# Kernel optimization log

Measured on AMD Instinct MI355X. Metric: run time of the kernel, lower is better.

## Reference

```python
import jax, jax.numpy as jnp
import numpy as np

N_EMBD = 1024
HEAD_SIZE = 64

def setup_inputs() -> dict:
    key = jax.random.key(0)
    kx, kk, kq, kv = jax.random.split(key, 4)
    x = jax.random.normal(kx, (8, 2048, N_EMBD), dtype=jnp.float32)
    # torch nn.Linear(n_embd, head_size, bias=False): y = x @ W.T, W:[head_size,n_embd].
    # We store the transposed form [n_embd, head_size] directly.
    s = 1.0 / np.sqrt(N_EMBD)
    Wk = jax.random.uniform(kk, (N_EMBD, HEAD_SIZE), jnp.float32, -s, s)
    Wq = jax.random.uniform(kq, (N_EMBD, HEAD_SIZE), jnp.float32, -s, s)
    Wv = jax.random.uniform(kv, (N_EMBD, HEAD_SIZE), jnp.float32, -s, s)
    return {"x": x, "Wk": Wk, "Wq": Wq, "Wv": Wv}

def reference(x, Wk, Wq, Wv):
    B, T, C = x.shape
    k = jnp.einsum('btc,cd->btd', x, Wk)  # [B,T,d]
    q = jnp.einsum('btc,cd->btd', x, Wq)
    v = jnp.einsum('btc,cd->btd', x, Wv)
    d = k.shape[-1]
    wei = jnp.einsum('btd,bsd->bts', q, k) * (d ** -0.5)  # [B,T,T]
    causal = jnp.tril(jnp.ones((T, T), dtype=bool))
    wei = jnp.where(causal, wei, -jnp.inf)
    wei = jax.nn.softmax(wei, axis=-1)
    # dropout p=0.0 -> identity (eval-mode equivalent)
    out = jnp.einsum('bts,bsd->btd', wei, v)  # [B,T,d]
    return out
```

## Files before the change

kernel.cpp:

```cpp
#include <hip/hip_runtime.h>
#include <hip/hip_bf16.h>

#define TB 8
#define TT 2048
#define TC 1024
#define TD 64
#define PSP 72

typedef __attribute__((ext_vector_type(8))) short bf16x8;
typedef __attribute__((ext_vector_type(4))) float f32x4;

__device__ __forceinline__ short f2bf(float f) {
    union { float f; unsigned u; } v; v.f = f;
    unsigned r = v.u + 0x7fffu + ((v.u >> 16) & 1u);
    return (short)(r >> 16);
}

__device__ __forceinline__ unsigned pk2(float a, float b) {
    __hip_bfloat162 h = __float22bfloat162_rn(make_float2(a, b));
    union { __hip_bfloat162 h2; unsigned u; } c; c.h2 = h;
    return c.u;
}

__device__ __forceinline__ void gl_lds16(const void* g, void* l) {
    __builtin_amdgcn_global_load_lds(
        (const __attribute__((address_space(1))) unsigned*)g,
        (__attribute__((address_space(3))) unsigned*)l, 16, 0, 0);
}

__device__ __forceinline__ void bar_raw() { asm volatile("s_barrier" ::: "memory"); }
#define WAIT_VM(n) asm volatile("s_waitcnt vmcnt(" #n ")" ::: "memory")

__global__ __launch_bounds__(256) void convert_w(const float* __restrict__ Wk,
                                                 const float* __restrict__ Wq,
                                                 const float* __restrict__ Wv,
                                                 short* __restrict__ Wt) {
    __shared__ short Tl[64 * PSP];
    const int tid = threadIdx.x;
    const int kc  = blockIdx.x;
    const int oid = blockIdx.y;
    const float* src = (oid == 0) ? Wk : (oid == 1) ? Wq : Wv;
    const float scale = (oid == 1) ? 0.125f : 1.0f;
    const int row = tid >> 2;
    const int c0  = (tid & 3) << 4;

    const float* sp = src + (size_t)(kc * 64 + row) * TD + c0;
    float4 a = ((const float4*)sp)[0], b = ((const float4*)sp)[1];
    float4 c = ((const float4*)sp)[2], d = ((const float4*)sp)[3];
    float vals[16] = {a.x,a.y,a.z,a.w, b.x,b.y,b.z,b.w,
                      c.x,c.y,c.z,c.w, d.x,d.y,d.z,d.w};
#pragma unroll
    for (int j = 0; j < 16; ++j)
        Tl[(c0 + j) * PSP + row] = f2bf(vals[j] * scale);
    __syncthreads();

    const int n  = tid >> 2;
    const int k0 = (tid & 3) << 4;
    uint4 u0 = *(uint4*)&Tl[n * PSP + k0];
    uint4 u1 = *(uint4*)&Tl[n * PSP + k0 + 8];
    uint4* dst = (uint4*)(Wt + (size_t)(oid * 64 + n) * TC + kc * 64 + k0);
    dst[0] = u0; dst[1] = u1;
}

__global__ __launch_bounds__(256, 1) void qkv_proj(const float* __restrict__ x,
                                                   const short* __restrict__ Wt,
                                                   short* __restrict__ qb,
                                                   short* __restrict__ kb,
                                                   short* __restrict__ vt) {
    __shared__ __align__(16) char sm[3 * 40960];
    const int tid = threadIdx.x;
    const int mg  = blockIdx.x;
    const int wv  = tid >> 6, lane = tid & 63;
    const int wu  = __builtin_amdgcn_readfirstlane(wv);
    const int l15 = lane & 15, quad = lane >> 4;

    f32x4 acc[12];
#pragma unroll
    for (int i = 0; i < 12; ++i) acc[i] = (f32x4){0.f, 0.f, 0.f, 0.f};

    const float* xtile = x + (size_t)mg * 64 * TC;

#define STAGE_Q(r)                                                          \
    {                                                                       \
        char* sb = sm + ((r) % 3) * 40960;                                  \
        float* xd = (float*)sb;                                             \
        short* wd = (short*)(sb + 16384);                                   \
        _Pragma("unroll")                                                   \
        for (int j = 0; j < 4; ++j) {                                       \
            int sbase = (j * 4 + wu) * 64;                                  \
            int sl = sbase + lane;                                          \
            int rw = sl >> 4, g = sl & 15;                                  \
            int gg = g ^ (rw & 15);                                         \
            gl_lds16(xtile + (size_t)rw * TC + (r) * 64 + gg * 4,           \
                     xd + (size_t)sbase * 4);                               \
        }                                                                   \
        _Pragma("unroll")                                                   \
        for (int j = 0; j < 6; ++j) {                                       \
            int n0 = (j * 4 + wu) * 8;                                      \
            int nb = n0 + (lane >> 3), g = lane & 7;                        \
            int gg = g ^ (nb & 7);                                          \
            gl_lds16(Wt + (size_t)nb * TC + (r) * 64 + gg * 8,              \
                     wd + (size_t)n0 * 64);                                 \
        }                                                                   \
    }

    STAGE_Q(0);
    STAGE_Q(1);
    for (int r = 0; r < 16; ++r) {
        if (r + 2 < 16)      { STAGE_Q(r + 2); WAIT_VM(20); }
        else if (r + 1 < 16) { WAIT_VM(10); }
        else                 { WAIT_VM(0); }
        bar_raw();
        const char* sb = sm + (r % 3) * 40960;
        const float* xb = (const float*)sb;
        const short* wb = (const short*)(sb + 16384);
        const int xrow = (wv * 16 + l15) * 16;
#pragma unroll
        for (int c = 0; c < 2; ++c) {
            int G = c * 8 + quad * 2;
            float4 f0 = *(const float4*)(xb + (xrow + (G ^ l15)) * 4);
            float4 f1 = *(const float4*)(xb + (xrow + ((G + 1) ^ l15)) * 4);
            union { bf16x8 v; unsigned u[4]; } pk;
            pk.u[0] = pk2(f0.x, f0.y); pk.u[1] = pk2(f0.z, f0.w);
            pk.u[2] = pk2(f1.x, f1.y); pk.u[3] = pk2(f1.z, f1.w);
#pragma unroll
            for (int nt = 0; nt < 12; ++nt) {
                bf16x8 B = *(const bf16x8*)(wb + (nt * 16 + l15) * 64
                                            + (((c * 4 + quad) ^ (l15 & 7)) * 8));
                acc[nt] = __builtin_amdgcn_mfma_f32_16x16x32_bf16(pk.v, B, acc[nt], 0, 0, 0);
            }
        }
        bar_raw();
    }
#undef STAGE_Q

    const int row0 = mg * 64;
    const int bb = row0 >> 11;
    const int m0 = wv * 16 + quad * 4;
#pragma unroll
    for (int nt = 0; nt < 4; ++nt)
#pragma unroll
        for (int rr = 0; rr < 4; ++rr)
            kb[(size_t)(row0 + m0 + rr) * TD + nt * 16 + l15] = f2bf(acc[nt][rr]);
#pragma unroll
    for (int nt = 4; nt < 8; ++nt)
#pragma unroll
        for (int rr = 0; rr < 4; ++rr)
            qb[(size_t)(row0 + m0 + rr) * TD + (nt - 4) * 16 + l15] = f2bf(acc[nt][rr]);
#pragma unroll
    for (int nt = 8; nt < 12; ++nt) {
        int d = (nt - 8) * 16 + l15;
        alignas(8) short t4[4];
#pragma unroll
        for (int rr = 0; rr < 4; ++rr) t4[rr] = f2bf(acc[nt][rr]);
        *(uint2*)(vt + (size_t)(bb * TD + d) * TT + (row0 & 2047) + m0) = *(uint2*)t4;
    }
}

__global__ __launch_bounds__(256, 1) void attn(const short* __restrict__ qb,
                                               const short* __restrict__ kb,
                                               const short* __restrict__ vt,
                                               float* __restrict__ out) {
    __shared__ __align__(16) char smem[107520];
    short* Ps = (short*)(smem + 98304);
    float* Os = (float*)smem;
    float* ls = (float*)(smem + 16384);

    const int tid = threadIdx.x;
    const int p   = blockIdx.x;
    const int b   = blockIdx.y;
    const int wv  = tid >> 6, lane = tid & 63;
    const int wu  = __builtin_amdgcn_readfirstlane(wv);
    const int l15 = lane & 15, quad = lane >> 4;
    const int qh  = wv >> 1;
    const int ks  = wv & 1;
    const float L2E = 1.4426950408889634f;

    const short* kbb = kb + (size_t)b * TT * TD;
    const short* vbb = vt + (size_t)b * TD * TT;
    short* myPs = Ps + wu * (16 * PSP);
    const int col = tid & 63;
    const int rb  = tid >> 6;

#define STAGE_KV(r, KTv)                                                    \
    {                                                                       \
        char* sb = smem + ((r) % 3) * 32768;                                \
        short* kdst = (short*)sb;                                           \
        short* vdst = (short*)(sb + 16384);                                 \
        _Pragma("unroll")                                                   \
        for (int h = 0; h < 2; ++h) {                                       \
            int kt = 2 * (r) + h; if (kt > (KTv) - 1) kt = (KTv) - 1;       \
            _Pragma("unroll")                                               \
            for (int j = 0; j < 2; ++j) {                                   \
                int sbase = (j * 4 + wu) * 64;                              \
                int sl = sbase + lane;                                      \
                int rw = sl >> 3, g = sl & 7;                               \
                int gg = g ^ (rw & 7);                                      \
                gl_lds16(kbb + (size_t)(kt * 64 + rw) * TD + gg * 8,        \
                         kdst + h * 4096 + sbase * 8);                      \
                gl_lds16(vbb + (size_t)rw * TT + kt * 64 + gg * 8,          \
                         vdst + h * 4096 + sbase * 8);                      \
            }                                                               \
        }                                                                   \
    }

    for (int phase = 0; phase < 2; ++phase) {
        const int it = phase ? (63 - p) : p;
        const int q0 = it * 32;
        const int KT = (it >> 1) + 1;
        const int R  = (KT + 1) >> 1;

        const size_t qoff = (size_t)(b * TT + q0 + qh * 16 + l15) * TD + quad * 8;
        bf16x8 aq0 = *(const bf16x8*)(qb + qoff);
        bf16x8 aq1 = *(const bf16x8*)(qb + qoff + 32);
        WAIT_VM(0);

        f32x4 O[4];
#pragma unroll
        for (int i = 0; i < 4; ++i) O[i] = (f32x4){0.f, 0.f, 0.f, 0.f};
        float lsum[4] = {0.f, 0.f, 0.f, 0.f};

        STAGE_KV(0, KT);
        if (1 < R) STAGE_KV(1, KT);
        for (int r = 0; r < R; ++r) {
            if (r + 2 < R)      { STAGE_KV(r + 2, KT); WAIT_VM(16); }
            else if (r + 1 < R) { WAIT_VM(8); }
            else                { WAIT_VM(0); }
            bar_raw();

            const int mykt = 2 * r + ks;
            if (mykt < KT) {
                const char* sb2 = (const char*)smem + (r % 3) * 32768;
                const short* Kt = (const short*)sb2 + ks * 4096;
                const short* Vt = (const short*)(sb2 + 16384) + ks * 4096;
                f32x4 S[4];
#pragma unroll
                for (int nt = 0; nt < 4; ++nt) {
                    int rw = nt * 16 + l15, r7 = l15 & 7;
                    bf16x8 b0 = *(const bf16x8*)(Kt + rw * 64 + (quad ^ r7) * 8);
                    bf16x8 b1 = *(const bf16x8*)(Kt + rw * 64 + ((4 + quad) ^ r7) * 8);
                    S[nt] = (f32x4){0.f, 0.f, 0.f, 0.f};
                    S[nt] = __builtin_amdgcn_mfma_f32_16x16x32_bf16(aq0, b0, S[nt], 0, 0, 0);
                    S[nt] = __builtin_amdgcn_mfma_f32_16x16x32_bf16(aq1, b1, S[nt], 0, 0, 0);
                }
                const bool diag = (mykt == KT - 1);
                const int qrow = q0 + qh * 16 + quad * 4;
#pragma unroll
                for (int nt = 0; nt < 4; ++nt) {
                    int scol = mykt * 64 + nt * 16 + l15;
#pragma unroll
                    for (int r4 = 0; r4 < 4; ++r4) {
                        float pv = exp2f(S[nt][r4] * L2E);
                        if (diag && (scol > qrow + r4)) pv = 0.f;
                        lsum[r4] += pv;
                        myPs[(quad * 4 + r4) * PSP + nt * 16 + l15] = f2bf(pv);
                    }
                }
                bf16x8 p0 = *(const bf16x8*)(myPs + l15 * PSP + quad * 8);
                bf16x8 p1 = *(const bf16x8*)(myPs + l15 * PSP + quad * 8 + 32);
#pragma unroll
                for (int dt = 0; dt < 4; ++dt) {
                    int rw = dt * 16 + l15, r7 = l15 & 7;
                    bf16x8 b0 = *(const bf16x8*)(Vt + rw * 64 + (quad ^ r7) * 8);
                    bf16x8 b1 = *(const bf16x8*)(Vt + rw * 64 + ((4 + quad) ^ r7) * 8);
                    O[dt] = __builtin_amdgcn_mfma_f32_16x16x32_bf16(p0, b0, O[dt], 0, 0, 0);
                    O[dt] = __builtin_amdgcn_mfma_f32_16x16x32_bf16(p1, b1, O[dt], 0, 0, 0);
                }
            }
            bar_raw();
        }
        __syncthreads();

#pragma unroll
        for (int r = 0; r < 4; ++r) {
            float v = lsum[r];
            v += __shfl_xor(v, 1); v += __shfl_xor(v, 2);
            v += __shfl_xor(v, 4); v += __shfl_xor(v, 8);
            lsum[r] = v;
        }
#pragma unroll
        for (int dt = 0; dt < 4; ++dt)
#pragma unroll
            for (int r = 0; r < 4; ++r)
                Os[(wv * 16 + quad * 4 + r) * 64 + dt * 16 + l15] = O[dt][r];
        if (l15 == 0)
#pragma unroll
            for (int r = 0; r < 4; ++r) ls[wv * 16 + quad * 4 + r] = lsum[r];
        __syncthreads();

        for (int rr = rb; rr < 32; rr += 4) {
            int h = rr >> 4, r16 = rr & 15;
            float o = Os[((2 * h)     * 16 + r16) * 64 + col]
                    + Os[((2 * h + 1) * 16 + r16) * 64 + col];
            float L = ls[(2 * h) * 16 + r16] + ls[(2 * h + 1) * 16 + r16];
            out[(size_t)(b * TT + q0 + rr) * TD + col] = o / L;
        }
        __syncthreads();
    }
#undef STAGE_KV
}

extern "C" void kernel_launch(void* const* d_in, const int* in_sizes, int n_in,
                              void* d_out, int out_size, void* d_ws, size_t ws_size,
                              hipStream_t stream) {
    const float* x  = (const float*)d_in[0];
    const float* Wk = (const float*)d_in[1];
    const float* Wq = (const float*)d_in[2];
    const float* Wv = (const float*)d_in[3];
    float* out = (float*)d_out;

    char* ws = (char*)d_ws;
    short* Wt = (short*)(ws);
    short* qb = (short*)(ws + 524288);
    short* kb = (short*)(ws + 2621440);
    short* vt = (short*)(ws + 4718592);

    convert_w<<<dim3(16, 3), dim3(256), 0, stream>>>(Wk, Wq, Wv, Wt);
    qkv_proj<<<dim3(256), dim3(256), 0, stream>>>(x, Wt, qb, kb, vt);
    attn<<<dim3(32, 8), dim3(256), 0, stream>>>(qb, kb, vt, out);
}
```

Before: 141.0 us.

## Restructure attention to one 64-row query tile per block, retile QKV warps

The attention kernel drops the paired-phase, split-K-across-waves scheme. Each block now handles one 64-query tile, with each wave owning 16 rows and the whole KV range. The separate LDS reduction of partial O and row sums goes away, and results are written directly to global memory. LDS use shrinks so two blocks can share a CU, and heavy tiles are scheduled first. The QKV projection switches to a 2x2 wave tiling, 32 rows by 6 n-tiles, so each B fragment is reused across two M tiles. It also gains a redundant first store loop with an odd index expression.

```diff
diff --git a/kernel.cpp b/kernel.cpp
--- a/kernel.cpp
+++ b/kernel.cpp
@@ -73,10 +73,14 @@
     const int wv  = tid >> 6, lane = tid & 63;
     const int wu  = __builtin_amdgcn_readfirstlane(wv);
     const int l15 = lane & 15, quad = lane >> 4;
-
-    f32x4 acc[12];
-#pragma unroll
-    for (int i = 0; i < 12; ++i) acc[i] = (f32x4){0.f, 0.f, 0.f, 0.f};
+    const int mh  = wv >> 1;
+    const int nh  = wv & 1;
+
+    f32x4 acc[2][6];
+#pragma unroll
+    for (int i = 0; i < 2; ++i)
+#pragma unroll
+        for (int j = 0; j < 6; ++j) acc[i][j] = (f32x4){0.f, 0.f, 0.f, 0.f};
 
     const float* xtile = x + (size_t)mg * 64 * TC;
 
@@ -114,190 +118,183 @@
         const char* sb = sm + (r % 3) * 40960;
         const float* xb = (const float*)sb;
         const short* wb = (const short*)(sb + 16384);
-        const int xrow = (wv * 16 + l15) * 16;
 #pragma unroll
         for (int c = 0; c < 2; ++c) {
             int G = c * 8 + quad * 2;
-            float4 f0 = *(const float4*)(xb + (xrow + (G ^ l15)) * 4);
-            float4 f1 = *(const float4*)(xb + (xrow + ((G + 1) ^ l15)) * 4);
-            union { bf16x8 v; unsigned u[4]; } pk;
-            pk.u[0] = pk2(f0.x, f0.y); pk.u[1] = pk2(f0.z, f0.w);
-            pk.u[2] = pk2(f1.x, f1.y); pk.u[3] = pk2(f1.z, f1.w);
-#pragma unroll
-            for (int nt = 0; nt < 12; ++nt) {
-                bf16x8 B = *(const bf16x8*)(wb + (nt * 16 + l15) * 64
-                                            + (((c * 4 + quad) ^ (l15 & 7)) * 8));
-                acc[nt] = __builtin_amdgcn_mfma_f32_16x16x32_bf16(pk.v, B, acc[nt], 0, 0, 0);
+#pragma unroll
+            for (int mt = 0; mt < 2; ++mt) {
+                const int xrow = (mh * 32 + mt * 16 + l15) * 16;
+                float4 f0 = *(const float4*)(xb + (xrow + (G ^ l15)) * 4);
+                float4 f1 = *(const float4*)(xb + (xrow + ((G + 1) ^ l15)) * 4);
+                union { bf16x8 v; unsigned u[4]; } pk;
+                pk.u[0] = pk2(f0.x, f0.y); pk.u[1] = pk2(f0.z, f0.w);
+                pk.u[2] = pk2(f1.x, f1.y); pk.u[3] = pk2(f1.z, f1.w);
+#pragma unroll
+                for (int i = 0; i < 6; ++i) {
+                    int nt = nh * 6 + i;
+                    bf16x8 B = *(const bf16x8*)(wb + (nt * 16 + l15) * 64
+                                                + (((c * 4 + quad) ^ (l15 & 7)) * 8));
+                    acc[mt][i] = __builtin_amdgcn_mfma_f32_16x16x32_bf16(
+                                     pk.v, B, acc[mt][i], 0, 0, 0);
+                }
             }
         }
         bar_raw();
     }
 #undef STAGE_Q
 
-    const int row0 = mg * 64;
-    const int bb = row0 >> 11;
-    const int m0 = wv * 16 + quad * 4;
-#pragma unroll
-    for (int nt = 0; nt < 4; ++nt)
-#pragma unroll
-        for (int rr = 0; rr < 4; ++rr)
-            kb[(size_t)(row0 + m0 + rr) * TD + nt * 16 + l15] = f2bf(acc[nt][rr]);
-#pragma unroll
-    for (int nt = 4; nt < 8; ++nt)
-#pragma unroll
-        for (int rr = 0; rr < 4; ++rr)
-            qb[(size_t)(row0 + m0 + rr) * TD + (nt - 4) * 16 + l15] = f2bf(acc[nt][rr]);
-#pragma unroll
-    for (int nt = 8; nt < 12; ++nt) {
-        int d = (nt - 8) * 16 + l15;
-        alignas(8) short t4[4];
-#pragma unroll
-        for (int rr = 0; rr < 4; ++rr) t4[rr] = f2bf(acc[nt][rr]);
-        *(uint2*)(vt + (size_t)(bb * TD + d) * TT + (row0 & 2047) + m0) = *(uint2*)t4;
-    }
-}
-
-__global__ __launch_bounds__(256, 1) void attn(const short* __restrict__ qb,
+    const int row0 = mg * 64 + mh * 32;
+    const int bb = mg >> 5;
+#pragma unroll
+    for (int i = 0; i < 6; ++i) {
+        int nt = nh * 6 + i;
+        if (nt < 4) {
+#pragma unroll
+            for (int mt = 0; mt < 2; ++mt)
+#pragma unroll
+                for (int rr = 0; rr < 4; ++rr)
+                    kb[(size_t)(row0 + mt * 16 + quad * 4 + rr) * TD + nt * 16 + l15]
+                        = f2bf(acc[mt][rr >> 2 ? 0 : i][rr]);
+        }
+    }
+#pragma unroll
+    for (int i = 0; i < 6; ++i) {
+        int nt = nh * 6 + i;
+#pragma unroll
+        for (int mt = 0; mt < 2; ++mt) {
+            if (nt < 4) {
+#pragma unroll
+                for (int rr = 0; rr < 4; ++rr)
+                    kb[(size_t)(row0 + mt * 16 + quad * 4 + rr) * TD + nt * 16 + l15]
+                        = f2bf(acc[mt][i][rr]);
+            } else if (nt < 8) {
+#pragma unroll
+                for (int rr = 0; rr < 4; ++rr)
+                    qb[(size_t)(row0 + mt * 16 + quad * 4 + rr) * TD + (nt - 4) * 16 + l15]
+                        = f2bf(acc[mt][i][rr]);
+            } else {
+                int d = (nt - 8) * 16 + l15;
+                alignas(8) short t4[4];
+#pragma unroll
+                for (int rr = 0; rr < 4; ++rr) t4[rr] = f2bf(acc[mt][i][rr]);
+                *(uint2*)(vt + (size_t)(bb * TD + d) * TT
+                          + ((row0 + mt * 16) & 2047) + quad * 4) = *(uint2*)t4;
+            }
+        }
+    }
+}
+
+__global__ __launch_bounds__(256, 2) void attn(const short* __restrict__ qb,
                                                const short* __restrict__ kb,
                                                const short* __restrict__ vt,
                                                float* __restrict__ out) {
-    __shared__ __align__(16) char smem[107520];
-    short* Ps = (short*)(smem + 98304);
-    float* Os = (float*)smem;
-    float* ls = (float*)(smem + 16384);
+    __shared__ __align__(16) char smem[58368];
+    short* Ps = (short*)(smem + 49152);
 
     const int tid = threadIdx.x;
-    const int p   = blockIdx.x;
-    const int b   = blockIdx.y;
+    const int pm  = blockIdx.x;
+    const int b   = pm & 7;
+    const int it  = 31 - (pm >> 3);
     const int wv  = tid >> 6, lane = tid & 63;
     const int wu  = __builtin_amdgcn_readfirstlane(wv);
     const int l15 = lane & 15, quad = lane >> 4;
-    const int qh  = wv >> 1;
-    const int ks  = wv & 1;
+    const int q0  = it * 64;
+    const int KT  = it + 1;
     const float L2E = 1.4426950408889634f;
 
     const short* kbb = kb + (size_t)b * TT * TD;
     const short* vbb = vt + (size_t)b * TD * TT;
     short* myPs = Ps + wu * (16 * PSP);
-    const int col = tid & 63;
-    const int rb  = tid >> 6;
-
-#define STAGE_KV(r, KTv)                                                    \
+
+    const size_t qoff = (size_t)(b * TT + q0 + wv * 16 + l15) * TD + quad * 8;
+    bf16x8 aq0 = *(const bf16x8*)(qb + qoff);
+    bf16x8 aq1 = *(const bf16x8*)(qb + qoff + 32);
+    WAIT_VM(0);
+
+    f32x4 O[4];
+#pragma unroll
+    for (int i = 0; i < 4; ++i) O[i] = (f32x4){0.f, 0.f, 0.f, 0.f};
+    float lsum[4] = {0.f, 0.f, 0.f, 0.f};
+
+#define STAGE_KV(r)                                                         \
     {                                                                       \
-        char* sb = smem + ((r) % 3) * 32768;                                \
-        short* kdst = (short*)sb;                                           \
-        short* vdst = (short*)(sb + 16384);                                 \
+        char* sb = smem + ((r) % 3) * 16384;                                \
+        short* kd = (short*)sb;                                             \
+        short* vd = (short*)(sb + 8192);                                    \
         _Pragma("unroll")                                                   \
-        for (int h = 0; h < 2; ++h) {                                       \
-            int kt = 2 * (r) + h; if (kt > (KTv) - 1) kt = (KTv) - 1;       \
-            _Pragma("unroll")                                               \
-            for (int j = 0; j < 2; ++j) {                                   \
-                int sbase = (j * 4 + wu) * 64;                              \
-                int sl = sbase + lane;                                      \
-                int rw = sl >> 3, g = sl & 7;                               \
-                int gg = g ^ (rw & 7);                                      \
-                gl_lds16(kbb + (size_t)(kt * 64 + rw) * TD + gg * 8,        \
-                         kdst + h * 4096 + sbase * 8);                      \
-                gl_lds16(vbb + (size_t)rw * TT + kt * 64 + gg * 8,          \
-                         vdst + h * 4096 + sbase * 8);                      \
-            }                                                               \
+        for (int j = 0; j < 2; ++j) {                                       \
+            int sbase = (j * 4 + wu) * 64;                                  \
+            int sl = sbase + lane;                                          \
+            int rw = sl >> 3, g = sl & 7;                                   \
+            int gg = g ^ (rw & 7);                                          \
+            gl_lds16(kbb + (size_t)((r) * 64 + rw) * TD + gg * 8,           \
+                     kd + sbase * 8);                                       \
+            gl_lds16(vbb + (size_t)rw * TT + (r) * 64 + gg * 8,             \
+                     vd + sbase * 8);                                       \
         }                                                                   \
     }
 
-    for (int phase = 0; phase < 2; ++phase) {
-        const int it = phase ? (63 - p) : p;
-        const int q0 = it * 32;
-        const int KT = (it >> 1) + 1;
-        const int R  = (KT + 1) >> 1;
-
-        const size_t qoff = (size_t)(b * TT + q0 + qh * 16 + l15) * TD + quad * 8;
-        bf16x8 aq0 = *(const bf16x8*)(qb + qoff);
-        bf16x8 aq1 = *(const bf16x8*)(qb + qoff + 32);
-        WAIT_VM(0);
-
-        f32x4 O[4];
-#pragma unroll
-        for (int i = 0; i < 4; ++i) O[i] = (f32x4){0.f, 0.f, 0.f, 0.f};
-        float lsum[4] = {0.f, 0.f, 0.f, 0.f};
-
-        STAGE_KV(0, KT);
-        if (1 < R) STAGE_KV(1, KT);
-        for (int r = 0; r < R; ++r) {
-            if (r + 2 < R)      { STAGE_KV(r + 2, KT); WAIT_VM(16); }
-            else if (r + 1 < R) { WAIT_VM(8); }
-            else                { WAIT_VM(0); }
-            bar_raw();
-
-            const int mykt = 2 * r + ks;
-            if (mykt < KT) {
-                const char* sb2 = (const char*)smem + (r % 3) * 32768;
-                const short* Kt = (const short*)sb2 + ks * 4096;
-                const short* Vt = (const short*)(sb2 + 16384) + ks * 4096;
-                f32x4 S[4];
-#pragma unroll
-                for (int nt = 0; nt < 4; ++nt) {
-                    int rw = nt * 16 + l15, r7 = l15 & 7;
-                    bf16x8 b0 = *(const bf16x8*)(Kt + rw * 64 + (quad ^ r7) * 8);
-                    bf16x8 b1 = *(const bf16x8*)(Kt + rw * 64 + ((4 + quad) ^ r7) * 8);
-                    S[nt] = (f32x4){0.f, 0.f, 0.f, 0.f};
-                    S[nt] = __builtin_amdgcn_mfma_f32_16x16x32_bf16(aq0, b0, S[nt], 0, 0, 0);
-                    S[nt] = __builtin_amdgcn_mfma_f32_16x16x32_bf16(aq1, b1, S[nt], 0, 0, 0);
-                }
-                const bool diag = (mykt == KT - 1);
-                const int qrow = q0 + qh * 16 + quad * 4;
-#pragma unroll
-                for (int nt = 0; nt < 4; ++nt) {
-                    int scol = mykt * 64 + nt * 16 + l15;
-#pragma unroll
-                    for (int r4 = 0; r4 < 4; ++r4) {
-                        float pv = exp2f(S[nt][r4] * L2E);
-                        if (diag && (scol > qrow + r4)) pv = 0.f;
-                        lsum[r4] += pv;
-                        myPs[(quad * 4 + r4) * PSP + nt * 16 + l15] = f2bf(pv);
-                    }
-                }
-                bf16x8 p0 = *(const bf16x8*)(myPs + l15 * PSP + quad * 8);
-                bf16x8 p1 = *(const bf16x8*)(myPs + l15 * PSP + quad * 8 + 32);
-#pragma unroll
-                for (int dt = 0; dt < 4; ++dt) {
-                    int rw = dt * 16 + l15, r7 = l15 & 7;
-                    bf16x8 b0 = *(const bf16x8*)(Vt + rw * 64 + (quad ^ r7) * 8);
-                    bf16x8 b1 = *(const bf16x8*)(Vt + rw * 64 + ((4 + quad) ^ r7) * 8);
-                    O[dt] = __builtin_amdgcn_mfma_f32_16x16x32_bf16(p0, b0, O[dt], 0, 0, 0);
-                    O[dt] = __builtin_amdgcn_mfma_f32_16x16x32_bf16(p1, b1, O[dt], 0, 0, 0);
-                }
+    STAGE_KV(0);
+    if (KT > 1) STAGE_KV(1);
+    for (int r = 0; r < KT; ++r) {
+        if (r + 2 < KT)      { STAGE_KV(r + 2); WAIT_VM(8); }
+        else if (r + 1 < KT) { WAIT_VM(4); }
+        else                 { WAIT_VM(0); }
+        bar_raw();
+
+        const char* sb2 = (const char*)smem + (r % 3) * 16384;
+        const short* Kt = (const short*)sb2;
+        const short* Vt = (const short*)(sb2 + 8192);
+        f32x4 S[4];
+#pragma unroll
+        for (int nt = 0; nt < 4; ++nt) {
+            int rw = nt * 16 + l15, r7 = l15 & 7;
+            bf16x8 b0 = *(const bf16x8*)(Kt + rw * 64 + (quad ^ r7) * 8);
+            bf16x8 b1 = *(const bf16x8*)(Kt + rw * 64 + ((4 + quad) ^ r7) * 8);
+            S[nt] = (f32x4){0.f, 0.f, 0.f, 0.f};
+            S[nt] = __builtin_amdgcn_mfma_f32_16x16x32_bf16(aq0, b0, S[nt], 0, 0, 0);
+            S[nt] = __builtin_amdgcn_mfma_f32_16x16x32_bf16(aq1, b1, S[nt], 0, 0, 0);
+        }
+        const bool diag = (r == KT - 1);
+        const int qrow = q0 + wv * 16 + quad * 4;
+#pragma unroll
+        for (int nt = 0; nt < 4; ++nt) {
+            int scol = r * 64 + nt * 16 + l15;
+#pragma unroll
+            for (int r4 = 0; r4 < 4; ++r4) {
+                float pv = exp2f(S[nt][r4] * L2E);
+                if (diag && (scol > qrow + r4)) pv = 0.f;
+                lsum[r4] += pv;
+                myPs[(quad * 4 + r4) * PSP + nt * 16 + l15] = f2bf(pv);
             }
-            bar_raw();
-        }
-        __syncthreads();
-
-#pragma unroll
-        for (int r = 0; r < 4; ++r) {
-            float v = lsum[r];
-            v += __shfl_xor(v, 1); v += __shfl_xor(v, 2);
-            v += __shfl_xor(v, 4); v += __shfl_xor(v, 8);
-            lsum[r] = v;
-        }
-#pragma unroll
-        for (int dt = 0; dt < 4; ++dt)
-#pragma unroll
-            for (int r = 0; r < 4; ++r)
-                Os[(wv * 16 + quad * 4 + r) * 64 + dt * 16 + l15] = O[dt][r];
-        if (l15 == 0)
-#pragma unroll
-            for (int r = 0; r < 4; ++r) ls[wv * 16 + quad * 4 + r] = lsum[r];
-        __syncthreads();
-
-        for (int rr = rb; rr < 32; rr += 4) {
-            int h = rr >> 4, r16 = rr & 15;
-            float o = Os[((2 * h)     * 16 + r16) * 64 + col]
-                    + Os[((2 * h + 1) * 16 + r16) * 64 + col];
-            float L = ls[(2 * h) * 16 + r16] + ls[(2 * h + 1) * 16 + r16];
-            out[(size_t)(b * TT + q0 + rr) * TD + col] = o / L;
-        }
-        __syncthreads();
+        }
+        bf16x8 p0 = *(const bf16x8*)(myPs + l15 * PSP + quad * 8);
+        bf16x8 p1 = *(const bf16x8*)(myPs + l15 * PSP + quad * 8 + 32);
+#pragma unroll
+        for (int dt = 0; dt < 4; ++dt) {
+            int rw = dt * 16 + l15, r7 = l15 & 7;
+            bf16x8 b0 = *(const bf16x8*)(Vt + rw * 64 + (quad ^ r7) * 8);
+            bf16x8 b1 = *(const bf16x8*)(Vt + rw * 64 + ((4 + quad) ^ r7) * 8);
+            O[dt] = __builtin_amdgcn_mfma_f32_16x16x32_bf16(p0, b0, O[dt], 0, 0, 0);
+            O[dt] = __builtin_amdgcn_mfma_f32_16x16x32_bf16(p1, b1, O[dt], 0, 0, 0);
+        }
+        bar_raw();
     }
 #undef STAGE_KV
+
+#pragma unroll
+    for (int r4 = 0; r4 < 4; ++r4) {
+        float v = lsum[r4];
+        v += __shfl_xor(v, 1); v += __shfl_xor(v, 2);
+        v += __shfl_xor(v, 4); v += __shfl_xor(v, 8);
+        lsum[r4] = v;
+    }
+#pragma unroll
+    for (int dt = 0; dt < 4; ++dt)
+#pragma unroll
+        for (int r4 = 0; r4 < 4; ++r4)
+            out[(size_t)(b * TT + q0 + wv * 16 + quad * 4 + r4) * TD + dt * 16 + l15]
+                = O[dt][r4] / lsum[r4];
 }
 
 extern "C" void kernel_launch(void* const* d_in, const int* in_sizes, int n_in,
@@ -317,5 +314,5 @@
 
     convert_w<<<dim3(16, 3), dim3(256), 0, stream>>>(Wk, Wq, Wv, Wt);
     qkv_proj<<<dim3(256), dim3(256), 0, stream>>>(x, Wt, qb, kb, vt);
-    attn<<<dim3(32, 8), dim3(256), 0, stream>>>(qb, kb, vt, out);
-}
+    attn<<<dim3(256), dim3(256), 0, stream>>>(qb, kb, vt, out);
+}
```

Result: no change. 143.8 us (+2.0%).
